# Performance work log

Hardware: AMD Instinct MI355X
Metric: run time of the kernel (lower is better)

## Reference

```python
import jax, jax.numpy as jnp
import numpy as np

N_PART = 2048
N_BINS = 16
N_FREQS = 8
N_BLOCKS = 4
N_HEADS = 8
DIM = 256
HID = 512
LOWER = 0.0
UPPER = 1.0
FIXED_IDXS = np.array([0, 1])
CHANGED_IDXS = np.array([2])
N_FIXED = 2
N_CHANGED = 1
EMB_IN = 2 * N_FREQS * N_FIXED + 3   # 35
AFF_OUT = N_CHANGED * (3 * N_BINS + 1)  # 49
MIN_BIN = 1e-4
MIN_SLOPE = 1e-4


def _mlp(x, W0, b0, W1, b1, W2, b2):
    # equinox MLP: depth=2 hidden layers, relu activation, identity final
    x = jax.nn.relu(x @ W0.T + b0)
    x = jax.nn.relu(x @ W1.T + b1)
    return x @ W2.T + b2


def _attention(x, Wq, Wk, bk, Wv, Wo, bo):
    # eqx.nn.MultiheadAttention: query bias off, key bias on, value bias off, output bias on
    S, D = x.shape
    dh = D // N_HEADS
    q = (x @ Wq.T).reshape(S, N_HEADS, dh)
    k = (x @ Wk.T + bk).reshape(S, N_HEADS, dh)
    v = (x @ Wv.T).reshape(S, N_HEADS, dh)
    logits = jnp.einsum('shd,thd->hst', q, k) / float(np.sqrt(dh))
    attn = jax.nn.softmax(logits, axis=-1)
    o = jnp.einsum('hst,thd->shd', attn, v).reshape(S, D)
    return o @ Wo.T + bo


def _circular(x, lower, upper, n_freqs):
    # periodic sin/cos embedding of coordinates on [lower, upper)
    freqs = 2.0 * jnp.pi * jnp.arange(1, n_freqs + 1, dtype=x.dtype) / (upper - lower)
    ang = (x - lower)[..., None] * freqs  # (rows, n_fixed, n_freqs)
    feats = jnp.concatenate([jnp.cos(ang), jnp.sin(ang)], axis=-1)
    return feats.reshape(x.shape[0], -1)  # (rows, 2*n_freqs*n_fixed)


def _rqs_forward(x, params):
    # distrax-style rational quadratic spline, boundary_slopes='circular'
    nb = N_BINS
    uw = params[..., :nb]
    uh = params[..., nb:2 * nb]
    ud = params[..., 2 * nb:]
    ud = jnp.concatenate([ud[..., :-1], ud[..., :1]], axis=-1)  # circular: last slope = first
    total = UPPER - LOWER
    widths = jax.nn.softmax(uw, axis=-1) * (total - nb * MIN_BIN) + MIN_BIN
    heights = jax.nn.softmax(uh, axis=-1) * (total - nb * MIN_BIN) + MIN_BIN
    offset = float(np.log(np.expm1(1.0 - MIN_SLOPE)))  # softplus(0+offset)+min = 1
    slopes = jax.nn.softplus(ud + offset) + MIN_SLOPE
    zero = jnp.zeros(widths.shape[:-1] + (1,), widths.dtype)
    xpos = LOWER + jnp.concatenate([zero, jnp.cumsum(widths, -1)], -1)   # (..., nb+1)
    ypos = LOWER + jnp.concatenate([zero, jnp.cumsum(heights, -1)], -1)
    inside = (x >= LOWER) & (x <= UPPER)
    xc = jnp.clip(x, LOWER, UPPER)
    k = jnp.clip(jnp.sum(xc[..., None] >= xpos, axis=-1) - 1, 0, nb - 1)
    g = lambda a: jnp.take_along_axis(a, k[..., None], axis=-1)[..., 0]
    xk, xk1 = g(xpos[..., :-1]), g(xpos[..., 1:])
    yk, yk1 = g(ypos[..., :-1]), g(ypos[..., 1:])
    dk, dk1 = g(slopes[..., :-1]), g(slopes[..., 1:])
    w = xk1 - xk
    h = yk1 - yk
    s = h / w
    z = (xc - xk) / w
    z1 = 1.0 - z
    den = s + (dk1 + dk - 2.0 * s) * z * z1
    y = yk + h * (s * z * z + dk * z * z1) / den
    logdet = 2.0 * jnp.log(s) + jnp.log(dk1 * z * z + 2.0 * s * z * z1 + dk * z1 * z1) - 2.0 * jnp.log(den)
    y = jnp.where(inside, y, x)
    logdet = jnp.where(inside, logdet, 0.0)
    return y, logdet


def _forward(pos, scale, press, temp,
             e_w0, e_b0, e_w1, e_b1, e_w2, e_b2,
             Wq, Wk, bk, Wv, Wo, bo,
             mw0, mb0, mw1, mb1, mw2, mb2,
             a_w0, a_b0, a_w1, a_b1, a_w2, a_b2):
    fixed = pos[1:, FIXED_IDXS]      # (N-1, 2)
    changed = pos[1:, CHANGED_IDXS]  # (N-1, 1)
    feats = _circular(fixed[:, FIXED_IDXS], LOWER, UPPER, N_FREQS)  # (N-1, 32)
    rows = feats.shape[0]
    ones = jnp.ones((rows, 1), feats.dtype)
    cond = jnp.concatenate([feats, ones * scale, ones * temp, ones * press], axis=-1)  # (N-1, 35)
    h = _mlp(cond, e_w0, e_b0, e_w1, e_b1, e_w2, e_b2)  # (N-1, DIM)
    for i in range(N_BLOCKS):
        h = h + _attention(h, Wq[i], Wk[i], bk[i], Wv[i], Wo[i], bo[i])
        h = h + _mlp(h, mw0[i], mb0[i], mw1[i], mb1[i], mw2[i], mb2[i])
    params = _mlp(h, a_w0, a_b0, a_w1, a_b1, a_w2, a_b2)
    params = params.reshape(N_PART - 1, N_CHANGED, 3 * N_BINS + 1)
    y, logdet = _rqs_forward(changed, params)
    pos = pos.at[1:, CHANGED_IDXS].set(y.reshape(N_PART - 1, N_CHANGED))
    return pos, logdet.sum()


def setup_inputs():
    kit = iter(jax.random.split(jax.random.key(0), 40))
    nk = lambda: next(kit)
    def W(out_d, in_d, pre=()):
        return jax.random.normal(nk(), pre + (out_d, in_d), jnp.float32) / np.sqrt(in_d)
    def b(out_d, pre=()):
        return 0.01 * jax.random.normal(nk(), pre + (out_d,), jnp.float32)
    B = (N_BLOCKS,)
    return dict(
        pos=jax.random.uniform(nk(), (N_PART, 3), jnp.float32),
        scale=jax.random.uniform(nk(), (), jnp.float32),
        press=jax.random.uniform(nk(), (), jnp.float32),
        temp=jax.random.uniform(nk(), (), jnp.float32),
        e_w0=W(HID, EMB_IN), e_b0=b(HID),
        e_w1=W(HID, HID), e_b1=b(HID),
        e_w2=W(DIM, HID), e_b2=b(DIM),
        Wq=W(DIM, DIM, B), Wk=W(DIM, DIM, B), bk=b(DIM, B),
        Wv=W(DIM, DIM, B), Wo=W(DIM, DIM, B), bo=b(DIM, B),
        mw0=W(HID, DIM, B), mb0=b(HID, B),
        mw1=W(HID, HID, B), mb1=b(HID, B),
        mw2=W(DIM, HID, B), mb2=b(DIM, B),
        a_w0=W(HID, DIM), a_b0=b(HID),
        a_w1=W(HID, HID), a_b1=b(HID),
        a_w2=W(AFF_OUT, HID), a_b2=b(AFF_OUT),
    )


def reference(pos, scale, press, temp,
              e_w0, e_b0, e_w1, e_b1, e_w2, e_b2,
              Wq, Wk, bk, Wv, Wo, bo,
              mw0, mb0, mw1, mb1, mw2, mb2,
              a_w0, a_b0, a_w1, a_b1, a_w2, a_b2):
    return _forward(pos, scale, press, temp,
                    e_w0, e_b0, e_w1, e_b1, e_w2, e_b2,
                    Wq, Wk, bk, Wv, Wo, bo,
                    mw0, mb0, mw1, mb1, mw2, mb2,
                    a_w0, a_b0, a_w1, a_b1, a_w2, a_b2)
```

## Files before the change

kernel.cpp:

```cpp
#include <hip/hip_runtime.h>
#include <math.h>

#define S_ROWS 2047
#define DIM 256
#define HID 512
#define NHEADS 8
#define DH 32
#define NBINS 16
#define AFF_OUT 49

typedef short bf16x8 __attribute__((ext_vector_type(8)));
typedef float f32x4 __attribute__((ext_vector_type(4)));
typedef float f32x16 __attribute__((ext_vector_type(16)));
typedef unsigned short u16x8 __attribute__((ext_vector_type(8)));
typedef unsigned short u16x4 __attribute__((ext_vector_type(4)));

__device__ inline unsigned short f2b(float f) {
    unsigned int u = __float_as_uint(f);
    u += 0x7FFFu + ((u >> 16) & 1u);
    return (unsigned short)(u >> 16);
}

#define W_MAIN 3957248
#define EW0P_N 32768
#define P0 (W_MAIN / 4)
#define P1 (P0 + EW0P_N / 4)
#define P2 (P1 + 2048 * 64 / 4)
#define P3 (P2 + 1537)
__global__ __launch_bounds__(256) void setup_kernel(
    const float* __restrict__ pos, const float* __restrict__ scale,
    const float* __restrict__ press, const float* __restrict__ temp,
    const float* __restrict__ e_w0, const float* __restrict__ p0,
    const float* __restrict__ p1, const float* __restrict__ p2,
    const float* __restrict__ p3, const float* __restrict__ p4,
    const float* __restrict__ p5, const float* __restrict__ p6,
    const float* __restrict__ p7, const float* __restrict__ p8,
    const float* __restrict__ p9, const float* __restrict__ p10,
    const float* __restrict__ p11, unsigned short* __restrict__ dst,
    unsigned short* __restrict__ cond, float* __restrict__ out)
{
    const int offs[13] = {0, 262144, 393216, 655360, 917504, 1179648, 1441792,
                          1966080, 3014656, 3538944, 3670016, 3932160, 3957248};
    const float* srcs[12] = {p0,p1,p2,p3,p4,p5,p6,p7,p8,p9,p10,p11};
    for (int i4 = blockIdx.x * blockDim.x + threadIdx.x; i4 < P3;
         i4 += gridDim.x * blockDim.x) {
        if (i4 < P0) {
            int e = i4 * 4;
            int s = 0;
            #pragma unroll
            for (int j = 1; j < 12; j++) s += (e >= offs[j]);
            const float4 v = *(const float4*)(srcs[s] + (e - offs[s]));
            u16x4 o;
            o[0] = f2b(v.x); o[1] = f2b(v.y); o[2] = f2b(v.z); o[3] = f2b(v.w);
            *(u16x4*)(dst + EW0P_N + e) = o;
        } else if (i4 < P1) {
            int e = (i4 - P0) * 4;
            u16x4 o;
            #pragma unroll
            for (int r = 0; r < 4; r++) {
                int ee = e + r;
                int row = ee >> 6, col = ee & 63;
                o[r] = (col < 35) ? f2b(e_w0[row * 35 + col]) : (unsigned short)0;
            }
            *(u16x4*)(dst + e) = o;
        } else if (i4 < P2) {
            int e = (i4 - P1) * 4;
            int row = e >> 6;
            u16x4 o;
            #pragma unroll
            for (int r = 0; r < 4; r++) {
                int c = (e + r) & 63;
                float v = 0.f;
                if (row < S_ROWS) {
                    if (c < 32) {
                        int coord = c >> 4;
                        int w = c & 15;
                        float x = pos[(row + 1) * 3 + coord];
                        float f = 6.283185307179586f * (float)((w & 7) + 1);
                        float ang = x * f;
                        v = (w < 8) ? cosf(ang) : sinf(ang);
                    } else if (c == 32) v = scale[0];
                    else if (c == 33) v = temp[0];
                    else if (c == 34) v = press[0];
                }
                o[r] = f2b(v);
            }
            *(u16x4*)(cond + e) = o;
        } else {
            int e = (i4 - P2) * 4;
            #pragma unroll
            for (int r = 0; r < 4; r++) {
                int ee = e + r;
                if (ee < 6144) out[ee] = pos[ee];
                else if (ee == 6144) out[ee] = 0.f;
            }
        }
    }
}

#define LDK 72
__global__ __launch_bounds__(256, 4) void gemm_bf16_64(
    const unsigned short* __restrict__ Ab, const unsigned short* __restrict__ W,
    const float* __restrict__ bias, const float* resF,
    float* Cf, unsigned short* Cb, int M, int K, int relu)
{
    __shared__ unsigned short As[32][LDK];
    __shared__ unsigned short Bs[32][LDK];
    int tid = threadIdx.x;
    int wave = tid >> 6, lane = tid & 63;
    int quad = lane >> 4, l16 = lane & 15;
    int rowf = (wave & 1) << 4, colf = (wave >> 1) << 4;
    int row0 = blockIdx.y << 5, col0 = blockIdx.x << 5;
    int srow = tid >> 3, scol = (tid & 7) << 3;

    f32x4 acc = {0.f, 0.f, 0.f, 0.f};

    const u16x8* ap = (const u16x8*)(Ab + (size_t)(row0 + srow) * K + scol);
    const u16x8* wp = (const u16x8*)(W + (size_t)(col0 + srow) * K + scol);
    u16x8 a0 = ap[0];
    u16x8 b0 = wp[0];

    for (int k0 = 0; k0 < K; k0 += 64) {
        *(u16x8*)&As[srow][scol] = a0;
        *(u16x8*)&Bs[srow][scol] = b0;
        __syncthreads();
        if (k0 + 64 < K) {
            ap += 8; wp += 8;
            a0 = ap[0]; b0 = wp[0];
        }
        #pragma unroll
        for (int kt = 0; kt < 64; kt += 32) {
            bf16x8 af = *(bf16x8*)&As[rowf + l16][kt + (quad << 3)];
            bf16x8 bf = *(bf16x8*)&Bs[colf + l16][kt + (quad << 3)];
            acc = __builtin_amdgcn_mfma_f32_16x16x32_bf16(af, bf, acc, 0, 0, 0);
        }
        __syncthreads();
    }
    int col = col0 + colf + l16;
    if (col < M) {
        float bv = bias ? bias[col] : 0.f;
        #pragma unroll
        for (int r = 0; r < 4; r++) {
            int row = row0 + rowf + (quad << 2) + r;
            if (row >= S_ROWS) continue;
            float v = acc[r] + bv;
            if (resF) v += resF[(size_t)row * M + col];
            if (relu) v = fmaxf(v, 0.f);
            if (Cf) Cf[(size_t)row * M + col] = v;
            if (Cb) Cb[(size_t)row * M + col] = f2b(v);
        }
    }
}

#define LDW 136
__global__ __launch_bounds__(256, 4) void gemm_bf16_128(
    const unsigned short* __restrict__ Ab, const unsigned short* __restrict__ W,
    const float* __restrict__ bias, const float* resF,
    float* Cf, unsigned short* Cb, int M, int K, int relu)
{
    __shared__ unsigned short As[32][LDW];
    __shared__ unsigned short Bs[32][LDW];
    int tid = threadIdx.x;
    int wave = tid >> 6, lane = tid & 63;
    int quad = lane >> 4, l16 = lane & 15;
    int rowf = (wave & 1) << 4, colf = (wave >> 1) << 4;
    int row0 = blockIdx.y << 5, col0 = blockIdx.x << 5;
    int srow = tid >> 3, scol = (tid & 7) << 4;

    f32x4 acc = {0.f, 0.f, 0.f, 0.f};

    const u16x8* ap = (const u16x8*)(Ab + (size_t)(row0 + srow) * K + scol);
    const u16x8* wp = (const u16x8*)(W + (size_t)(col0 + srow) * K + scol);
    u16x8 a0 = ap[0], a1 = ap[1];
    u16x8 b0 = wp[0], b1 = wp[1];

    for (int k0 = 0; k0 < K; k0 += 128) {
        *(u16x8*)&As[srow][scol]     = a0;
        *(u16x8*)&As[srow][scol + 8] = a1;
        *(u16x8*)&Bs[srow][scol]     = b0;
        *(u16x8*)&Bs[srow][scol + 8] = b1;
        __syncthreads();
        if (k0 + 128 < K) {
            ap += 16; wp += 16;
            a0 = ap[0]; a1 = ap[1];
            b0 = wp[0]; b1 = wp[1];
        }
        #pragma unroll
        for (int kt = 0; kt < 128; kt += 32) {
            bf16x8 af = *(bf16x8*)&As[rowf + l16][kt + (quad << 3)];
            bf16x8 bf = *(bf16x8*)&Bs[colf + l16][kt + (quad << 3)];
            acc = __builtin_amdgcn_mfma_f32_16x16x32_bf16(af, bf, acc, 0, 0, 0);
        }
        __syncthreads();
    }
    int col = col0 + colf + l16;
    if (col < M) {
        float bv = bias ? bias[col] : 0.f;
        #pragma unroll
        for (int r = 0; r < 4; r++) {
            int row = row0 + rowf + (quad << 2) + r;
            if (row >= S_ROWS) continue;
            float v = acc[r] + bv;
            if (resF) v += resF[(size_t)row * M + col];
            if (relu) v = fmaxf(v, 0.f);
            if (Cf) Cf[(size_t)row * M + col] = v;
            if (Cb) Cb[(size_t)row * M + col] = f2b(v);
        }
    }
}

__global__ __launch_bounds__(256, 4) void gemm_qkv(
    const unsigned short* __restrict__ Ab, const unsigned short* __restrict__ Wq,
    const unsigned short* __restrict__ Wk, const unsigned short* __restrict__ Wv,
    const float* __restrict__ bk,
    unsigned short* __restrict__ qbh, unsigned short* __restrict__ kbh,
    unsigned short* __restrict__ vbT)
{
    __shared__ unsigned short As[32][LDW];
    __shared__ unsigned short Bs[32][LDW];
    const int N = S_ROWS, K = 256;
    int tid = threadIdx.x;
    int wave = tid >> 6, lane = tid & 63;
    int quad = lane >> 4, l16 = lane & 15;
    int rowf = (wave & 1) << 4, colf = (wave >> 1) << 4;
    int row0 = blockIdx.y << 5, col0 = blockIdx.x << 5;
    int mode = col0 >> 8;
    int wcol0 = col0 & 255;
    const unsigned short* W = (mode == 0) ? Wq : (mode == 1) ? Wk : Wv;
    int srow = tid >> 3, scol = (tid & 7) << 4;

    f32x4 acc = {0.f, 0.f, 0.f, 0.f};

    const u16x8* ap = (const u16x8*)(Ab + (size_t)(row0 + srow) * K + scol);
    const u16x8* wp = (const u16x8*)(W + (size_t)(wcol0 + srow) * K + scol);
    u16x8 a0 = ap[0], a1 = ap[1];
    u16x8 b0 = wp[0], b1 = wp[1];

    for (int k0 = 0; k0 < K; k0 += 128) {
        *(u16x8*)&As[srow][scol]     = a0;
        *(u16x8*)&As[srow][scol + 8] = a1;
        *(u16x8*)&Bs[srow][scol]     = b0;
        *(u16x8*)&Bs[srow][scol + 8] = b1;
        __syncthreads();
        if (k0 + 128 < K) {
            ap += 16; wp += 16;
            a0 = ap[0]; a1 = ap[1];
            b0 = wp[0]; b1 = wp[1];
        }
        #pragma unroll
        for (int kt = 0; kt < 128; kt += 32) {
            bf16x8 af = *(bf16x8*)&As[rowf + l16][kt + (quad << 3)];
            bf16x8 bf = *(bf16x8*)&Bs[colf + l16][kt + (quad << 3)];
            acc = __builtin_amdgcn_mfma_f32_16x16x32_bf16(af, bf, acc, 0, 0, 0);
        }
        __syncthreads();
    }
    int colr = wcol0 + colf + l16;
    int hh = colr >> 5, d = colr & 31;
    int rbase = row0 + rowf + (quad << 2);
    if (mode == 2) {
        unsigned short* dst = vbT + ((size_t)hh * 32 + d) * 2048 + rbase;
        if (rbase + 3 < N) {
            u16x4 o;
            #pragma unroll
            for (int r = 0; r < 4; r++) o[r] = f2b(acc[r]);
            *(u16x4*)dst = o;
        } else {
            #pragma unroll
            for (int r = 0; r < 4; r++)
                if (rbase + r < N) dst[r] = f2b(acc[r]);
        }
    } else {
        float bias = (mode == 1) ? bk[colr] : 0.f;
        unsigned short* dst = ((mode == 0) ? qbh : kbh) + (size_t)hh * 2048 * 32 + d;
        #pragma unroll
        for (int r = 0; r < 4; r++) {
            int row = rbase + r;
            if (row < N) {
                float v = acc[r] + bias;
                if (mode == 0) v *= 0.25506362f;
                dst[(size_t)row * 32] = f2b(v);
            }
        }
    }
}

__global__ __launch_bounds__(512, 2) void attn_mfma(
    const unsigned short* __restrict__ qbh,
    const unsigned short* __restrict__ kbh,
    const unsigned short* __restrict__ vbT,
    unsigned short* __restrict__ obb)
{
    int tid = threadIdx.x;
    int w = tid >> 6;
    int lane = tid & 63;
    int l31 = lane & 31, hf = lane >> 5;
    int q0 = blockIdx.x << 5;
    int h = blockIdx.y;
    int kstart = w * 256;
    int kend = min(kstart + 256, S_ROWS);

    const unsigned short* qp = qbh + ((size_t)h * 2048 + (q0 + l31)) * 32 + hf * 8;
    bf16x8 qf0 = *(const bf16x8*)(qp);
    bf16x8 qf1 = *(const bf16x8*)(qp + 16);

    const unsigned short* kb_h = kbh + (size_t)h * 2048 * 32;
    const unsigned short* vb_h = vbT + ((size_t)h * 32 + l31) * 2048;

    f32x16 acc = {};
    float m = -1e30f, l = 0.f;

    for (int key0 = kstart; key0 < kend; key0 += 32) {
        const unsigned short* kp = kb_h + (size_t)(key0 + l31) * 32 + hf * 8;
        bf16x8 kf0 = *(const bf16x8*)(kp);
        bf16x8 kf1 = *(const bf16x8*)(kp + 16);
        bf16x8 vf0 = *(const bf16x8*)(vb_h + key0 + hf * 8);
        bf16x8 vf1 = *(const bf16x8*)(vb_h + key0 + 16 + hf * 8);

        f32x16 sc = {};
        sc = __builtin_amdgcn_mfma_f32_32x32x16_bf16(kf0, qf0, sc, 0, 0, 0);
        sc = __builtin_amdgcn_mfma_f32_32x32x16_bf16(kf1, qf1, sc, 0, 0, 0);

        if (key0 + 32 > kend) {
            #pragma unroll
            for (int r = 0; r < 16; r++) {
                int kr = key0 + (r & 3) + 8 * (r >> 2) + 4 * hf;
                if (kr >= kend) sc[r] = -1e30f;
            }
        }
        float tmax = sc[0];
        #pragma unroll
        for (int r = 1; r < 16; r++) tmax = fmaxf(tmax, sc[r]);
        tmax = fmaxf(tmax, __shfl_xor(tmax, 32, 64));
        float mnew = fmaxf(m, tmax);
        float corr = __builtin_amdgcn_exp2f(m - mnew);
        m = mnew;
        float p[16];
        float ls = 0.f;
        #pragma unroll
        for (int r = 0; r < 16; r++) {
            p[r] = __builtin_amdgcn_exp2f(sc[r] - mnew);
            ls += p[r];
        }
        ls += __shfl_xor(ls, 32, 64);
        l = l * corr + ls;
        if (__ballot(corr != 1.0f)) {
            #pragma unroll
            for (int r = 0; r < 16; r++) acc[r] *= corr;
        }
        unsigned int pk[8];
        #pragma unroll
        for (int i = 0; i < 8; i++)
            pk[i] = __builtin_amdgcn_perm(__float_as_uint(p[2*i+1]),
                                          __float_as_uint(p[2*i]), 0x07060302u);
        unsigned int x[8];
        #pragma unroll
        for (int i = 0; i < 8; i++)
            x[i] = (unsigned int)__shfl_xor((int)pk[i], 32, 64);
        union { unsigned int u[4]; bf16x8 v; } B1, B2;
        B1.u[0] = hf ? x[2]  : pk[0];
        B1.u[1] = hf ? x[3]  : pk[1];
        B1.u[2] = hf ? pk[2] : x[0];
        B1.u[3] = hf ? pk[3] : x[1];
        B2.u[0] = hf ? x[6]  : pk[4];
        B2.u[1] = hf ? x[7]  : pk[5];
        B2.u[2] = hf ? pk[6] : x[4];
        B2.u[3] = hf ? pk[7] : x[5];
        acc = __builtin_amdgcn_mfma_f32_32x32x16_bf16(vf0, B1.v, acc, 0, 0, 0);
        acc = __builtin_amdgcn_mfma_f32_32x32x16_bf16(vf1, B2.v, acc, 0, 0, 0);
    }

    __shared__ float sm_m[8][32];
    __shared__ float sm_l[8][32];
    __shared__ float sm_acc[8][32][36];
    if (!hf) { sm_m[w][l31] = m; sm_l[w][l31] = l; }
    #pragma unroll
    for (int g = 0; g < 4; g++) {
        float4 o4;
        o4.x = acc[4*g]; o4.y = acc[4*g+1]; o4.z = acc[4*g+2]; o4.w = acc[4*g+3];
        *(float4*)&sm_acc[w][l31][8*g + 4*hf] = o4;
    }
    __syncthreads();

    if (tid < 256) {
        int q = tid & 31;
        int dg = tid >> 5;
        float mmax = -1e30f;
        #pragma unroll
        for (int c = 0; c < 8; c++) mmax = fmaxf(mmax, sm_m[c][q]);
        float lsum = 0.f;
        float num0 = 0.f, num1 = 0.f, num2 = 0.f, num3 = 0.f;
        #pragma unroll
        for (int c = 0; c < 8; c++) {
            float wgt = __builtin_amdgcn_exp2f(sm_m[c][q] - mmax);
            lsum += sm_l[c][q] * wgt;
            float4 o4 = *(const float4*)&sm_acc[c][q][dg * 4];
            num0 = fmaf(o4.x, wgt, num0);
            num1 = fmaf(o4.y, wgt, num1);
            num2 = fmaf(o4.z, wgt, num2);
            num3 = fmaf(o4.w, wgt, num3);
        }
        float inv = 1.f / lsum;
        if (q0 + q < S_ROWS) {
            u16x4 st;
            st[0] = f2b(num0 * inv); st[1] = f2b(num1 * inv);
            st[2] = f2b(num2 * inv); st[3] = f2b(num3 * inv);
            *(u16x4*)(obb + (size_t)(q0 + q) * DIM + h * DH + dg * 4) = st;
        }
    }
}

__global__ __launch_bounds__(64) void spline_kernel(const float* __restrict__ pos,
    const float* __restrict__ params, float* __restrict__ out)
{
    int r = blockIdx.x * 64 + threadIdx.x;
    float ld = 0.f;
    if (r < S_ROWS) {
        const float* p = params + (size_t)r * AFF_OUT;
        float x = pos[(r + 1) * 3 + 2];
        float xc = fminf(fmaxf(x, 0.f), 1.f);

        float mw = -1e30f, mh = -1e30f;
        #pragma unroll
        for (int j = 0; j < NBINS; j++) {
            mw = fmaxf(mw, p[j]);
            mh = fmaxf(mh, p[NBINS + j]);
        }
        float sw = 0.f, sh = 0.f;
        #pragma unroll
        for (int j = 0; j < NBINS; j++) {
            sw += __expf(p[j] - mw);
            sh += __expf(p[NBINS + j] - mh);
        }
        const float span = 1.0f - NBINS * 1e-4f;
        float scw = span / sw, sch = span / sh;

        float cumw = 0.f, cumh = 0.f;
        float xk = 0.f, yk = 0.f, wk = 0.f, hk = 0.f;
        int k = 0;
        #pragma unroll
        for (int j = 0; j < NBINS; j++) {
            float wj = __expf(p[j] - mw) * scw + 1e-4f;
            float hj = __expf(p[NBINS + j] - mh) * sch + 1e-4f;
            if (xc >= cumw) { k = j; xk = cumw; yk = cumh; wk = wj; hk = hj; }
            cumw += wj; cumh += hj;
        }
        float offset = logf(expm1f(0.9999f));
        float t0 = p[2 * NBINS + k] + offset;
        float t1 = ((k == NBINS - 1) ? p[2 * NBINS] : p[2 * NBINS + k + 1]) + offset;
        float dk  = ((t0 > 15.f) ? t0 : log1pf(__expf(t0))) + 1e-4f;
        float dk1 = ((t1 > 15.f) ? t1 : log1pf(__expf(t1))) + 1e-4f;

        float sl = hk / wk;
        float z = (xc - xk) / wk;
        float z1 = 1.f - z;
        float den = sl + (dk1 + dk - 2.f * sl) * z * z1;
        float y = yk + hk * (sl * z * z + dk * z * z1) / den;
        float ldv = 2.f * logf(sl)
                  + logf(dk1 * z * z + 2.f * sl * z * z1 + dk * z1 * z1)
                  - 2.f * logf(den);
        bool inside = (x >= 0.f) && (x <= 1.f);
        y = inside ? y : x;
        ld = inside ? ldv : 0.f;
        out[(r + 1) * 3 + 2] = y;
    }
    #pragma unroll
    for (int st = 32; st > 0; st >>= 1) ld += __shfl_xor(ld, st, 64);
    if (threadIdx.x == 0) atomicAdd(&out[6144], ld);
}

extern "C" void kernel_launch(void* const* d_in, const int* in_sizes, int n_in,
                              void* d_out, int out_size, void* d_ws, size_t ws_size,
                              hipStream_t stream)
{
    const float* pos   = (const float*)d_in[0];
    const float* scale = (const float*)d_in[1];
    const float* press = (const float*)d_in[2];
    const float* temp  = (const float*)d_in[3];
    const float* e_w0  = (const float*)d_in[4];
    const float* e_b0  = (const float*)d_in[5];
    const float* e_w1  = (const float*)d_in[6];
    const float* e_b1  = (const float*)d_in[7];
    const float* e_w2  = (const float*)d_in[8];
    const float* e_b2  = (const float*)d_in[9];
    const float* Wq    = (const float*)d_in[10];
    const float* Wk    = (const float*)d_in[11];
    const float* bk    = (const float*)d_in[12];
    const float* Wv    = (const float*)d_in[13];
    const float* Wo    = (const float*)d_in[14];
    const float* bo    = (const float*)d_in[15];
    const float* mw0   = (const float*)d_in[16];
    const float* mb0   = (const float*)d_in[17];
    const float* mw1   = (const float*)d_in[18];
    const float* mb1   = (const float*)d_in[19];
    const float* mw2   = (const float*)d_in[20];
    const float* mb2   = (const float*)d_in[21];
    const float* a_w0  = (const float*)d_in[22];
    const float* a_b0  = (const float*)d_in[23];
    const float* a_w1  = (const float*)d_in[24];
    const float* a_b1  = (const float*)d_in[25];
    const float* a_w2  = (const float*)d_in[26];
    const float* a_b2  = (const float*)d_in[27];
    float* out = (float*)d_out;

    enum { OFF_EW0 = 0,
           OFF_EW1 = 32768 + 0,       OFF_EW2 = 32768 + 262144,
           OFF_WQ  = 32768 + 393216,  OFF_WK  = 32768 + 655360,
           OFF_WV  = 32768 + 917504,  OFF_WO  = 32768 + 1179648,
           OFF_MW0 = 32768 + 1441792, OFF_MW1 = 32768 + 1966080,
           OFF_MW2 = 32768 + 3014656, OFF_AW0 = 32768 + 3538944,
           OFF_AW1 = 32768 + 3670016, OFF_AW2 = 32768 + 3932160 };
    const size_t WB_U16 = (size_t)EW0P_N + W_MAIN;

    float* ws = (float*)d_ws;
    size_t off = 0;
    float* hbuf = ws + off; off += 2048 * 256;
    float* pr   = ws + off; off += 2048 * 64;
    unsigned short* wbp   = (unsigned short*)(ws + off); off += WB_U16 / 2;
    unsigned short* cond  = (unsigned short*)(ws + off); off += 2048 * 64 / 2;
    unsigned short* t1b   = (unsigned short*)(ws + off); off += 2048 * 512 / 2;
    unsigned short* t2b   = (unsigned short*)(ws + off); off += 2048 * 512 / 2;
    unsigned short* hb    = (unsigned short*)(ws + off); off += 2048 * 256 / 2;
    unsigned short* obb   = (unsigned short*)(ws + off); off += 2048 * 256 / 2;
    unsigned short* qbh   = (unsigned short*)(ws + off); off += NHEADS * 2048 * 32 / 2;
    unsigned short* kbh   = (unsigned short*)(ws + off); off += NHEADS * 2048 * 32 / 2;
    unsigned short* vbT   = (unsigned short*)(ws + off); off += NHEADS * 2048 * 32 / 2;
    (void)ws_size;

    hipLaunchKernelGGL(setup_kernel, dim3(1024), dim3(256), 0, stream,
                       pos, scale, press, temp, e_w0,
                       e_w1, e_w2, Wq, Wk, Wv, Wo, mw0, mw1, mw2,
                       a_w0, a_w1, a_w2, wbp, cond, out);

    auto gemm = [&](const unsigned short* A, const unsigned short* W,
                    const float* bias, const float* resF, float* Cf,
                    unsigned short* Cb, int M, int K, int relu) {
        dim3 grid((M + 31) / 32, 64);
        if (K % 128 == 0)
            hipLaunchKernelGGL(gemm_bf16_128, grid, dim3(256), 0, stream,
                               A, W, bias, resF, Cf, Cb, M, K, relu);
        else
            hipLaunchKernelGGL(gemm_bf16_64, grid, dim3(256), 0, stream,
                               A, W, bias, resF, Cf, Cb, M, K, relu);
    };

    gemm(cond, wbp + OFF_EW0, e_b0, nullptr, nullptr, t1b, 512, 64, 1);
    gemm(t1b,  wbp + OFF_EW1, e_b1, nullptr, nullptr, t2b, 512, 512, 1);
    gemm(t2b,  wbp + OFF_EW2, e_b2, nullptr, hbuf, hb, 256, 512, 0);

    for (int l = 0; l < 4; l++) {
        hipLaunchKernelGGL(gemm_qkv, dim3(24, 64), dim3(256), 0, stream,
                           hb, wbp + OFF_WQ + l * 65536, wbp + OFF_WK + l * 65536,
                           wbp + OFF_WV + l * 65536, bk + l * 256, qbh, kbh, vbT);
        hipLaunchKernelGGL(attn_mfma, dim3(64, NHEADS), dim3(512), 0, stream,
                           qbh, kbh, vbT, obb);
        gemm(obb, wbp + OFF_WO + l * 65536, bo + l * 256, hbuf, hbuf, hb, 256, 256, 0);
        gemm(hb,  wbp + OFF_MW0 + l * 131072, mb0 + l * 512, nullptr, nullptr, t1b, 512, 256, 1);
        gemm(t1b, wbp + OFF_MW1 + l * 262144, mb1 + l * 512, nullptr, nullptr, t2b, 512, 512, 1);
        gemm(t2b, wbp + OFF_MW2 + l * 131072, mb2 + l * 256, hbuf, hbuf, hb, 256, 512, 0);
    }

    gemm(hb,  wbp + OFF_AW0, a_b0, nullptr, nullptr, t1b, 512, 256, 1);
    gemm(t1b, wbp + OFF_AW1, a_b1, nullptr, nullptr, t2b, 512, 512, 1);
    gemm(t2b, wbp + OFF_AW2, a_b2, nullptr, pr, nullptr, AFF_OUT, 512, 0);

    hipLaunchKernelGGL(spline_kernel, dim3(32), dim3(64), 0, stream, pos, pr, out);
}
```

Before: 338.9 us.

## Fuse final affine MLP chain and spline into one kernel

Replaces the three separate affine-head GEMM launches and the spline launch with a single kernel. Each 256-thread block takes 8 rows, keeps the intermediate activations in LDS, and runs the three MFMA stages followed by the spline. The aim is to save three launches plus the global round-trips of the intermediates. In exchange, each block reloads the full weight matrices from global/L2, and the 8-row tiles leave half of each 16-row MFMA tile unused.

```diff
diff --git a/kernel.cpp b/kernel.cpp
--- a/kernel.cpp
+++ b/kernel.cpp
@@ -410,63 +410,160 @@
     }
 }
 
-__global__ __launch_bounds__(64) void spline_kernel(const float* __restrict__ pos,
-    const float* __restrict__ params, float* __restrict__ out)
-{
-    int r = blockIdx.x * 64 + threadIdx.x;
-    float ld = 0.f;
-    if (r < S_ROWS) {
-        const float* p = params + (size_t)r * AFF_OUT;
-        float x = pos[(r + 1) * 3 + 2];
-        float xc = fminf(fmaxf(x, 0.f), 1.f);
-
-        float mw = -1e30f, mh = -1e30f;
-        #pragma unroll
-        for (int j = 0; j < NBINS; j++) {
-            mw = fmaxf(mw, p[j]);
-            mh = fmaxf(mh, p[NBINS + j]);
-        }
-        float sw = 0.f, sh = 0.f;
-        #pragma unroll
-        for (int j = 0; j < NBINS; j++) {
-            sw += __expf(p[j] - mw);
-            sh += __expf(p[NBINS + j] - mh);
-        }
-        const float span = 1.0f - NBINS * 1e-4f;
-        float scw = span / sw, sch = span / sh;
-
-        float cumw = 0.f, cumh = 0.f;
-        float xk = 0.f, yk = 0.f, wk = 0.f, hk = 0.f;
-        int k = 0;
-        #pragma unroll
-        for (int j = 0; j < NBINS; j++) {
-            float wj = __expf(p[j] - mw) * scw + 1e-4f;
-            float hj = __expf(p[NBINS + j] - mh) * sch + 1e-4f;
-            if (xc >= cumw) { k = j; xk = cumw; yk = cumh; wk = wj; hk = hj; }
-            cumw += wj; cumh += hj;
-        }
-        float offset = logf(expm1f(0.9999f));
-        float t0 = p[2 * NBINS + k] + offset;
-        float t1 = ((k == NBINS - 1) ? p[2 * NBINS] : p[2 * NBINS + k + 1]) + offset;
-        float dk  = ((t0 > 15.f) ? t0 : log1pf(__expf(t0))) + 1e-4f;
-        float dk1 = ((t1 > 15.f) ? t1 : log1pf(__expf(t1))) + 1e-4f;
-
-        float sl = hk / wk;
-        float z = (xc - xk) / wk;
-        float z1 = 1.f - z;
-        float den = sl + (dk1 + dk - 2.f * sl) * z * z1;
-        float y = yk + hk * (sl * z * z + dk * z * z1) / den;
-        float ldv = 2.f * logf(sl)
-                  + logf(dk1 * z * z + 2.f * sl * z * z1 + dk * z1 * z1)
-                  - 2.f * logf(den);
-        bool inside = (x >= 0.f) && (x <= 1.f);
-        y = inside ? y : x;
-        ld = inside ? ldv : 0.f;
-        out[(r + 1) * 3 + 2] = y;
-    }
+__device__ __forceinline__ float spline_row(const float* p, float x, float* yout)
+{
+    float xc = fminf(fmaxf(x, 0.f), 1.f);
+    float mw = -1e30f, mh = -1e30f;
     #pragma unroll
-    for (int st = 32; st > 0; st >>= 1) ld += __shfl_xor(ld, st, 64);
-    if (threadIdx.x == 0) atomicAdd(&out[6144], ld);
+    for (int j = 0; j < NBINS; j++) {
+        mw = fmaxf(mw, p[j]);
+        mh = fmaxf(mh, p[NBINS + j]);
+    }
+    float sw = 0.f, shs = 0.f;
+    #pragma unroll
+    for (int j = 0; j < NBINS; j++) {
+        sw += __expf(p[j] - mw);
+        shs += __expf(p[NBINS + j] - mh);
+    }
+    const float span = 1.0f - NBINS * 1e-4f;
+    float scw = span / sw, sch = span / shs;
+    float cumw = 0.f, cumh = 0.f;
+    float xk = 0.f, yk = 0.f, wk = 0.f, hk = 0.f;
+    int k = 0;
+    #pragma unroll
+    for (int j = 0; j < NBINS; j++) {
+        float wj = __expf(p[j] - mw) * scw + 1e-4f;
+        float hj = __expf(p[NBINS + j] - mh) * sch + 1e-4f;
+        if (xc >= cumw) { k = j; xk = cumw; yk = cumh; wk = wj; hk = hj; }
+        cumw += wj; cumh += hj;
+    }
+    float offset = logf(expm1f(0.9999f));
+    float t0 = p[2 * NBINS + k] + offset;
+    float t1 = ((k == NBINS - 1) ? p[2 * NBINS] : p[2 * NBINS + k + 1]) + offset;
+    float dk  = ((t0 > 15.f) ? t0 : log1pf(__expf(t0))) + 1e-4f;
+    float dk1 = ((t1 > 15.f) ? t1 : log1pf(__expf(t1))) + 1e-4f;
+    float sl = hk / wk;
+    float z = (xc - xk) / wk;
+    float z1 = 1.f - z;
+    float den = sl + (dk1 + dk - 2.f * sl) * z * z1;
+    float y = yk + hk * (sl * z * z + dk * z * z1) / den;
+    float ldv = 2.f * logf(sl)
+              + logf(dk1 * z * z + 2.f * sl * z * z1 + dk * z1 * z1)
+              - 2.f * logf(den);
+    bool inside = (x >= 0.f) && (x <= 1.f);
+    *yout = inside ? y : x;
+    return inside ? ldv : 0.f;
+}
+
+#define LDA 520
+
+template<int K, int M, bool RELU>
+__device__ __forceinline__ void aff_stage(
+    const unsigned short (*IN)[LDA], unsigned short (*OUT)[LDA],
+    const unsigned short* __restrict__ W, const float* __restrict__ bias,
+    int wv, int quad, int l16)
+{
+    constexpr int NI = K / 32;
+    bf16x8 af[NI];
+    #pragma unroll
+    for (int i = 0; i < NI; i++)
+        af[i] = *(const bf16x8*)&IN[l16 & 7][(i << 5) + (quad << 3)];
+    #pragma unroll
+    for (int p = 0; p < M / 64; p++) {
+        int col = (p << 6) + (wv << 4) + l16;
+        const unsigned short* wp = W + (size_t)col * K + (quad << 3);
+        f32x4 acc = {0.f, 0.f, 0.f, 0.f};
+        #pragma unroll
+        for (int kc = 0; kc < K / 256; kc++) {
+            bf16x8 w[8];
+            #pragma unroll
+            for (int j = 0; j < 8; j++)
+                w[j] = *(const bf16x8*)(wp + (kc << 8) + (j << 5));
+            #pragma unroll
+            for (int j = 0; j < 8; j++)
+                acc = __builtin_amdgcn_mfma_f32_16x16x32_bf16(
+                          af[(kc << 3) + j], w[j], acc, 0, 0, 0);
+        }
+        if (quad < 2) {
+            float bv = bias[col];
+            #pragma unroll
+            for (int r = 0; r < 4; r++) {
+                float v = acc[r] + bv;
+                if (RELU) v = fmaxf(v, 0.f);
+                OUT[(quad << 2) + r][col] = f2b(v);
+            }
+        }
+    }
+}
+
+__global__ __launch_bounds__(256) void aff_chain_kernel(
+    const unsigned short* __restrict__ hb,
+    const unsigned short* __restrict__ wbp_aw0,
+    const unsigned short* __restrict__ wbp_aw1,
+    const unsigned short* __restrict__ wbp_aw2,
+    const float* __restrict__ a_b0, const float* __restrict__ a_b1,
+    const float* __restrict__ a_b2,
+    const float* __restrict__ pos, float* __restrict__ out)
+{
+    __shared__ unsigned short actA[8][LDA];
+    __shared__ unsigned short actB[8][LDA];
+    __shared__ float pl[8][52];
+
+    int tid = threadIdx.x;
+    int wv = tid >> 6, lane = tid & 63;
+    int quad = lane >> 4, l16 = lane & 15;
+    int row0 = blockIdx.x << 3;
+
+    {
+        int r = tid >> 5, c = (tid & 31) << 3;
+        *(u16x8*)&actA[r][c] = *(const u16x8*)(hb + (size_t)(row0 + r) * 256 + c);
+    }
+    __syncthreads();
+    aff_stage<256, 512, true>(actA, actB, wbp_aw0, a_b0, wv, quad, l16);
+    __syncthreads();
+    aff_stage<512, 512, true>(actB, actA, wbp_aw1, a_b1, wv, quad, l16);
+    __syncthreads();
+    {
+        bf16x8 af[16];
+        #pragma unroll
+        for (int i = 0; i < 16; i++)
+            af[i] = *(const bf16x8*)&actA[l16 & 7][(i << 5) + (quad << 3)];
+        int col = (wv << 4) + l16;
+        int wr = (col < AFF_OUT) ? col : (AFF_OUT - 1);
+        const unsigned short* wp = wbp_aw2 + (size_t)wr * 512 + (quad << 3);
+        f32x4 acc = {0.f, 0.f, 0.f, 0.f};
+        #pragma unroll
+        for (int kc = 0; kc < 2; kc++) {
+            bf16x8 w[8];
+            #pragma unroll
+            for (int j = 0; j < 8; j++)
+                w[j] = *(const bf16x8*)(wp + (kc << 8) + (j << 5));
+            #pragma unroll
+            for (int j = 0; j < 8; j++)
+                acc = __builtin_amdgcn_mfma_f32_16x16x32_bf16(
+                          af[(kc << 3) + j], w[j], acc, 0, 0, 0);
+        }
+        if (quad < 2 && col < AFF_OUT) {
+            float bv = a_b2[col];
+            #pragma unroll
+            for (int r = 0; r < 4; r++)
+                pl[(quad << 2) + r][col] = acc[r] + bv;
+        }
+    }
+    __syncthreads();
+    if (tid < 8) {
+        float ld = 0.f;
+        int grow = row0 + tid;
+        if (grow < S_ROWS) {
+            float x = pos[(grow + 1) * 3 + 2];
+            float y;
+            ld = spline_row(&pl[tid][0], x, &y);
+            out[(grow + 1) * 3 + 2] = y;
+        }
+        #pragma unroll
+        for (int st = 4; st > 0; st >>= 1) ld += __shfl_xor(ld, st, 64);
+        if (tid == 0) atomicAdd(&out[6144], ld);
+    }
 }
 
 extern "C" void kernel_launch(void* const* d_in, const int* in_sizes, int n_in,
@@ -515,7 +612,6 @@
     float* ws = (float*)d_ws;
     size_t off = 0;
     float* hbuf = ws + off; off += 2048 * 256;
-    float* pr   = ws + off; off += 2048 * 64;
     unsigned short* wbp   = (unsigned short*)(ws + off); off += WB_U16 / 2;
     unsigned short* cond  = (unsigned short*)(ws + off); off += 2048 * 64 / 2;
     unsigned short* t1b   = (unsigned short*)(ws + off); off += 2048 * 512 / 2;
@@ -560,9 +656,7 @@
         gemm(t2b, wbp + OFF_MW2 + l * 131072, mb2 + l * 256, hbuf, hbuf, hb, 256, 512, 0);
     }
 
-    gemm(hb,  wbp + OFF_AW0, a_b0, nullptr, nullptr, t1b, 512, 256, 1);
-    gemm(t1b, wbp + OFF_AW1, a_b1, nullptr, nullptr, t2b, 512, 512, 1);
-    gemm(t2b, wbp + OFF_AW2, a_b2, nullptr, pr, nullptr, AFF_OUT, 512, 0);
-
-    hipLaunchKernelGGL(spline_kernel, dim3(32), dim3(64), 0, stream, pos, pr, out);
-}
+    hipLaunchKernelGGL(aff_chain_kernel, dim3(256), dim3(256), 0, stream,
+                       hb, wbp + OFF_AW0, wbp + OFF_AW1, wbp + OFF_AW2,
+                       a_b0, a_b1, a_b2, pos, out);
+}
```

Result: slower. 353.4 us (+4.3%).
